# Kernel optimization log

Measured on AMD Instinct MI355X. Metric: run time of the kernel, lower is better.

The kernel has to match this reference:

```python
import jax, jax.numpy as jnp
import numpy as np

# ---- config (matches init_kwargs) ----
B, N_ENC, COND_REPEAT = 4, 4, 200
BLOCKS, LAYERS_PER = 2, 8
R, S, CC, CLASSES = 128, 128, 64, 256
Q_ZERO = 128
DILATIONS = [2 ** i for i in range(LAYERS_PER)] * BLOCKS  # [1..128, 1..128]
L = len(DILATIONS)


def setup_inputs() -> dict:
    key = jax.random.key(0)
    ks = jax.random.split(key, 12)
    g = lambda k, shape, fan: (jax.random.normal(k, shape, jnp.float32) / np.float32(np.sqrt(fan)))
    return {
        "encodings": jax.random.normal(ks[0], (B, CC, N_ENC), jnp.float32),
        "W_first": g(ks[1], (R, 1, 2), 2.0),            # causal conv 1->R, k=2
        "b_first": jnp.zeros((R,), jnp.float32),
        "Wc": g(ks[2], (L, 2 * R, R, 2), 2.0 * R),       # dilated causal convs R->2R, k=2
        "bc": jnp.zeros((L, 2 * R), jnp.float32),
        "Wcond": g(ks[3], (L, 2 * R, CC), CC),           # per-layer 1x1 cond (no bias)
        "Wres": g(ks[4], (L, R, R), R),                  # per-layer 1x1 residual
        "bres": jnp.zeros((L, R), jnp.float32),
        "Wskip_l": g(ks[5], (L, S, R), R),               # per-layer 1x1 skip
        "bskip_l": jnp.zeros((L, S), jnp.float32),
        "Wskip0": g(ks[6], (S, R), R),                   # top skip_conv
        "bskip0": jnp.zeros((S,), jnp.float32),
        "Wcond_top": g(ks[7], (S, CC), CC),              # top 1x1 cond (no bias)
        "Wfc": g(ks[8], (S, S), S),
        "bfc": jnp.zeros((S,), jnp.float32),
        "Wlogits": g(ks[9], (CLASSES, S), S),
        "blogits": jnp.zeros((CLASSES,), jnp.float32),
    }


def reference(encodings, W_first, b_first, Wc, bc, Wcond, Wres, bres,
              Wskip_l, bskip_l, Wskip0, bskip0, Wcond_top, Wfc, bfc,
              Wlogits, blogits):
    """Autoregressive WaveNet generation with per-layer dilated-conv queues.
    Returns per-step logits [B, CLASSES, T] (sampling uses argmax, method='max')."""
    T = N_ENC * COND_REPEAT
    # each encoding frame conditions cond_repeat consecutive samples
    c_seq = jnp.repeat(encodings, COND_REPEAT, axis=2).transpose(2, 0, 1)  # [T,B,CC]

    def step(carry, c_t):
        sample, fq, queues = carry  # sample:[B] int, fq:[B] (first-conv queue), queues: tuple of [B,R,d_l]
        x = sample.astype(jnp.float32) / 127.5 - 1.0  # mu-law index -> [-1, 1]
        # first causal conv (k=2): past value from queue, current value x
        res = fq[:, None] * W_first[:, 0, 0] + x[:, None] * W_first[:, 0, 1] + b_first  # [B,R]
        skip = res @ Wskip0.T + bskip0  # [B,S]
        new_queues = []
        for l in range(L):  # fixed structural loop over layers
            q = queues[l]  # [B,R,d_l]; q[:,:,0] is the input from d_l steps ago
            z = q[:, :, 0] @ Wc[l, :, :, 0].T + res @ Wc[l, :, :, 1].T + bc[l]  # [B,2R]
            z = z + c_t @ Wcond[l].T
            gate, out = jnp.split(z, 2, axis=1)
            h = jax.nn.sigmoid(gate) * jnp.tanh(out)
            new_queues.append(jnp.concatenate([q[:, :, 1:], res[:, :, None]], axis=2))
            skip = skip + h @ Wskip_l[l].T + bskip_l[l]
            res = res + h @ Wres[l].T + bres[l]  # residual connection
        s = jax.nn.relu(skip) @ Wfc.T + bfc + c_t @ Wcond_top.T
        logits = jax.nn.relu(s) @ Wlogits.T + blogits  # [B,CLASSES]
        new_sample = jnp.argmax(logits, axis=1).astype(jnp.int32)
        return (new_sample, x, tuple(new_queues)), logits

    carry0 = (jnp.full((B,), Q_ZERO, jnp.int32),
              jnp.zeros((B,), jnp.float32),
              tuple(jnp.zeros((B, R, d), jnp.float32) for d in DILATIONS))
    _, logits = jax.lax.scan(step, carry0, c_seq)
    return logits.transpose(1, 2, 0)  # [B, CLASSES, T]
```

## Files before the change

kernel.cpp:

```cpp
#include <hip/hip_runtime.h>


typedef unsigned long long u64;

#define TSTEPS 800
#define CREP 200

#define CTR_OFF 0
#define ABT_OFF 64
#define RESBOX_OFF 4096
#define BOXB 16384
#define SKIPBOX_OFF (RESBOX_OFF + 4 * BOXB)
#define RING_OFF (SKIPBOX_OFF + 4 * BOXB)
#define RINGB 261120
#define WS_END (RING_OFF + 4 * RINGB)

#define SPIN_LIMIT 1048576

static __device__ __forceinline__ void pub64(u64* p, float x, unsigned tag) {
  const u64 v = (u64)__float_as_uint(x) | ((u64)tag << 32);
  asm volatile("global_atomic_swap_x2 %0, %1, off" ::"v"(p), "v"(v) : "memory");
}
static __device__ __forceinline__ u64 poll64(u64* p) {
  u64 old;
  const u64 z = 0;
  asm volatile("global_atomic_add_x2 %0, %1, %2, off sc0\n\ts_waitcnt vmcnt(0)"
               : "=&v"(old) : "v"(p), "v"(z) : "memory");
  return old;
}
static __device__ __forceinline__ void poll4(u64* p, u64& a, u64& b, u64& c, u64& d) {
  const u64 z = 0;
  asm volatile(
      "global_atomic_add_x2 %0, %4, %5, off sc0\n\t"
      "global_atomic_add_x2 %1, %4, %5, off offset:1024 sc0\n\t"
      "global_atomic_add_x2 %2, %4, %5, off offset:2048 sc0\n\t"
      "global_atomic_add_x2 %3, %4, %5, off offset:3072 sc0\n\t"
      "s_waitcnt vmcnt(0)"
      : "=&v"(a), "=&v"(b), "=&v"(c), "=&v"(d)
      : "v"(p), "v"(z)
      : "memory");
}
static __device__ __forceinline__ unsigned ld32(const unsigned* p) {
  return __hip_atomic_load(p, __ATOMIC_RELAXED, __HIP_MEMORY_SCOPE_AGENT);
}
static __device__ __forceinline__ void st32(unsigned* p, unsigned v) {
  __hip_atomic_store(p, v, __ATOMIC_RELAXED, __HIP_MEMORY_SCOPE_AGENT);
}
static __device__ __forceinline__ float spinf(u64* p, unsigned tag, unsigned* abt) {
  int g = 0;
  for (;;) {
    const u64 v = poll64(p);
    if ((unsigned)(v >> 32) == tag) return __uint_as_float((unsigned)v);
    if (((++g) & 255) == 0) {
      if (g > SPIN_LIMIT || ld32(abt)) { st32(abt, 1u); return 0.f; }
    }
  }
}

__global__ void wn_init(unsigned char* ws) {
  uint4 z; z.x = 0; z.y = 0; z.z = 0; z.w = 0;
  uint4* p = (uint4*)ws;
  const int n = WS_END / 16;
  for (int i = blockIdx.x * blockDim.x + threadIdx.x; i < n; i += gridDim.x * blockDim.x)
    p[i] = z;
}

__global__ __launch_bounds__(256, 1) void wn_main(
    const float* __restrict__ enc, const float* __restrict__ Wfirst,
    const float* __restrict__ bfirst, const float* __restrict__ Wc,
    const float* __restrict__ bcv, const float* __restrict__ Wcond,
    const float* __restrict__ Wres, const float* __restrict__ bres,
    const float* __restrict__ Wskip, const float* __restrict__ bskipl,
    const float* __restrict__ Wskip0, const float* __restrict__ bskip0,
    const float* __restrict__ Wct, const float* __restrict__ Wfcw,
    const float* __restrict__ bfc, const float* __restrict__ Wlg,
    const float* __restrict__ blgg, float* __restrict__ dout,
    unsigned char* __restrict__ ws) {
  __shared__ __attribute__((aligned(16))) unsigned char smem[8192];
  float* zbS = (float*)smem;
  float* ct2 = (float*)smem;
  float* res0S = (float*)(smem + 2048);
  float* skS = (float*)(smem + 2560);
  float* s1S = (float*)(smem + 3072);
  float* resS = (float*)(smem + 4096);
  float* zS = (float*)(smem + 4608);
  float* hS = (float*)(smem + 5632);
  float* partS = (float*)(smem + 6144);
  float* amaxv = (float*)(smem + 7168);
  int* amaxi = (int*)(smem + 7184);
  int* argixS = (int*)(smem + 7200);
  int* roleS = (int*)(smem + 7216);
  float* pastS = (float*)(smem + 7424);

  const int tid = threadIdx.x;
  unsigned* abt = (unsigned*)(ws + ABT_OFF);

  if (tid == 0) {
    unsigned xcc;
    asm volatile("s_getreg_b32 %0, hwreg(HW_REG_XCC_ID)" : "=s"(xcc));
    int role = 999;
    if (xcc < 4)
      role = (int)__hip_atomic_fetch_add((unsigned*)(ws + CTR_OFF) + xcc, 1u,
                                         __ATOMIC_RELAXED, __HIP_MEMORY_SCOPE_AGENT);
    roleS[0] = role;
    roleS[1] = (int)xcc;
  }
  __syncthreads();
  const int role = roleS[0];
  const int b = roleS[1];
  if (role >= 17) return;

  const int j2 = tid & 127, kh = tid >> 7;

  if (role < 16) {
    const int l = role;
    const int dl = 1 << (l & 7);
    const int pfx = (l < 8) ? ((1 << l) - 1) : (254 + (1 << (l - 8)));

    float wc1r[128], wresr[64];
#pragma unroll
    for (int k = 0; k < 64; k++) {
      const float4 v = ((const float4*)Wc)[(size_t)(l * 256 + tid) * 64 + k];
      wc1r[2 * k] = v.y; wc1r[2 * k + 1] = v.w;
    }
#pragma unroll
    for (int k = 0; k < 16; k++) {
      const float4 v = ((const float4*)(Wres + (size_t)(l * 128 + j2) * 128 + kh * 64))[k];
      wresr[4 * k] = v.x; wresr[4 * k + 1] = v.y; wresr[4 * k + 2] = v.z; wresr[4 * k + 3] = v.w;
    }
    const float bresv = bres[l * 128 + j2];

    for (int e = 0; e < 4; e++) {
      float a = bcv[l * 256 + tid];
      for (int c = 0; c < 64; c++)
        a = fmaf(enc[(b * 64 + c) * 4 + e], Wcond[((size_t)l * 256 + tid) * 64 + c], a);
      zbS[e * 256 + tid] = a;
    }

    u64* inbox = (u64*)(ws + RESBOX_OFF + (size_t)b * BOXB) + l * 128;
    u64* outbox = (u64*)(ws + RESBOX_OFF + (size_t)b * BOXB) + ((l + 1) & 15) * 128;
    u64* skipbox = (u64*)(ws + SKIPBOX_OFF + (size_t)b * BOXB) + l * 128;
    float* ringf = (float*)(ws + RING_OFF + (size_t)b * RINGB) + pfx * 128;
    float pp = 0.f;
    __syncthreads();

    for (int t = 0; t < TSTEPS; t++) {
      const unsigned want = (unsigned)(t + 1);
      const int e = t / CREP;

      if (tid < 128) resS[tid] = spinf(inbox + tid, want, abt);
      __syncthreads();

      float z = pp + zbS[e * 256 + tid];
      {
        const float4* r4 = (const float4*)resS;
#pragma unroll
        for (int k = 0; k < 32; k++) {
          const float4 r = r4[k];
          z = fmaf(r.x, wc1r[4 * k], z);
          z = fmaf(r.y, wc1r[4 * k + 1], z);
          z = fmaf(r.z, wc1r[4 * k + 2], z);
          z = fmaf(r.w, wc1r[4 * k + 3], z);
        }
      }
      zS[tid] = z;
      __syncthreads();
      if (tid < 128) {
        const float g = zS[tid], o = zS[tid + 128];
        hS[tid] = (1.f / (1.f + expf(-g))) * tanhf(o);
      }
      __syncthreads();

      if (l < 15) {
        const float4* h4 = (const float4*)(hS + kh * 64);
        float p = 0.f;
#pragma unroll
        for (int k = 0; k < 16; k++) {
          const float4 hv = h4[k];
          p = fmaf(hv.x, wresr[4 * k], p);
          p = fmaf(hv.y, wresr[4 * k + 1], p);
          p = fmaf(hv.z, wresr[4 * k + 2], p);
          p = fmaf(hv.w, wresr[4 * k + 3], p);
        }
        partS[tid] = p;
        __syncthreads();
        if (tid < 128)
          pub64(outbox + tid, resS[tid] + partS[tid] + partS[tid + 128] + bresv, want);
        __syncthreads();
      }


      {
        const float4* wr = (const float4*)(Wskip + (size_t)(l * 128 + j2) * 128 + kh * 64);
        const float4* h4 = (const float4*)(hS + kh * 64);
        float p = 0.f;
#pragma unroll
        for (int k = 0; k < 16; k++) {
          const float4 wv = wr[k];
          const float4 hv = h4[k];
          p = fmaf(wv.x, hv.x, p);
          p = fmaf(wv.y, hv.y, p);
          p = fmaf(wv.z, hv.z, p);
          p = fmaf(wv.w, hv.w, p);
        }
        partS[tid] = p;
      }
      __syncthreads();
      if (tid < 128) pub64(skipbox + tid, partS[tid] + partS[tid + 128], want);

      if (tid < 128) {
        ringf[(t % dl) * 128 + tid] = resS[tid];
        pastS[tid] = (dl == 1) ? resS[tid] : ringf[((t + 1) % dl) * 128 + tid];
      }
      __syncthreads();
      {
        const float4* wv4 = (const float4*)(Wc + (size_t)(l * 256 + tid) * 256);
        float p2 = 0.f;
#pragma unroll 8
        for (int k = 0; k < 64; k++) {
          const float4 v = wv4[k];
          p2 = fmaf(pastS[2 * k], v.x, p2);
          p2 = fmaf(pastS[2 * k + 1], v.z, p2);
        }
        pp = p2;
      }
    }
  } else {
    float wfcr[64], wlgr[128];
#pragma unroll
    for (int k = 0; k < 16; k++) {
      const float4 v = ((const float4*)(Wfcw + (size_t)j2 * 128 + kh * 64))[k];
      wfcr[4 * k] = v.x; wfcr[4 * k + 1] = v.y; wfcr[4 * k + 2] = v.z; wfcr[4 * k + 3] = v.w;
    }
#pragma unroll
    for (int k = 0; k < 32; k++) {
      const float4 v = ((const float4*)(Wlg + (size_t)tid * 128))[k];
      wlgr[4 * k] = v.x; wlgr[4 * k + 1] = v.y; wlgr[4 * k + 2] = v.z; wlgr[4 * k + 3] = v.w;
    }
    const float wf0 = Wfirst[2 * j2], wf1 = Wfirst[2 * j2 + 1], bfv = bfirst[j2];
    const float bs0 = bskip0[j2];
    float bsum = 0.f;
    for (int l2 = 0; l2 < 16; l2++) bsum += bskipl[l2 * 128 + j2];
    const float bfcv = bfc[j2];
    const float blgv = blgg[tid];
    if (tid < 128) {
      for (int e = 0; e < 4; e++) {
        float a = 0.f;
        for (int c = 0; c < 64; c++)
          a = fmaf(enc[(b * 64 + c) * 4 + e], Wct[tid * 64 + c], a);
        ct2[e * 128 + tid] = a;
      }
    }
    float fq = 0.f, x = 128.f / 127.5f - 1.f;
    u64* res0box = (u64*)(ws + RESBOX_OFF + (size_t)b * BOXB);
    u64* skb = (u64*)(ws + SKIPBOX_OFF + (size_t)b * BOXB);
    __syncthreads();

    for (int t = 0; t < TSTEPS; t++) {
      const unsigned want = (unsigned)(t + 1);
      const int e = t / CREP;

      if (tid < 128) {
        const float rv = fmaf(fq, wf0, fmaf(x, wf1, bfv));
        pub64(res0box + tid, rv, want);
        res0S[tid] = rv;
      }
      __syncthreads();

      {
        const float4* wr = (const float4*)(Wskip0 + (size_t)j2 * 128 + kh * 64);
        const float4* h4 = (const float4*)(res0S + kh * 64);
        float p = 0.f;
#pragma unroll
        for (int k = 0; k < 16; k++) {
          const float4 wv = wr[k];
          const float4 hv = h4[k];
          p = fmaf(wv.x, hv.x, p);
          p = fmaf(wv.y, hv.y, p);
          p = fmaf(wv.z, hv.z, p);
          p = fmaf(wv.w, hv.w, p);
        }
        partS[tid] = p;
      }
      __syncthreads();
      if (tid < 128) {
        float sacc = partS[tid] + partS[tid + 128] + bs0 + bsum;
        u64 v[16];
        int g = 0;
        for (;;) {
          bool ok = true;
#pragma unroll
          for (int grp = 0; grp < 4; grp++)
            poll4(skb + grp * 512 + tid, v[grp * 4], v[grp * 4 + 1], v[grp * 4 + 2], v[grp * 4 + 3]);
#pragma unroll
          for (int l2 = 0; l2 < 16; l2++) ok &= ((unsigned)(v[l2] >> 32) == want);
          if (ok) break;
          if (((++g) & 63) == 0) {
            if (g > (SPIN_LIMIT >> 6) || ld32(abt)) { st32(abt, 1u); break; }
          }
        }
#pragma unroll
        for (int l2 = 0; l2 < 16; l2++) sacc += __uint_as_float((unsigned)v[l2]);
        skS[tid] = fmaxf(sacc, 0.f);
      }
      __syncthreads();

      {
        const float4* h4 = (const float4*)(skS + kh * 64);
        float p = 0.f;
#pragma unroll
        for (int k = 0; k < 16; k++) {
          const float4 hv = h4[k];
          p = fmaf(hv.x, wfcr[4 * k], p);
          p = fmaf(hv.y, wfcr[4 * k + 1], p);
          p = fmaf(hv.z, wfcr[4 * k + 2], p);
          p = fmaf(hv.w, wfcr[4 * k + 3], p);
        }
        partS[tid] = p;
      }
      __syncthreads();
      if (tid < 128)
        s1S[tid] = fmaxf(partS[tid] + partS[tid + 128] + bfcv + ct2[e * 128 + tid], 0.f);
      __syncthreads();

      float lg = blgv;
      {
        const float4* h4 = (const float4*)s1S;
#pragma unroll
        for (int k = 0; k < 32; k++) {
          const float4 hv = h4[k];
          lg = fmaf(hv.x, wlgr[4 * k], lg);
          lg = fmaf(hv.y, wlgr[4 * k + 1], lg);
          lg = fmaf(hv.z, wlgr[4 * k + 2], lg);
          lg = fmaf(hv.w, wlgr[4 * k + 3], lg);
        }
      }

      float bv = lg;
      int bi = tid;
#pragma unroll
      for (int off = 32; off >= 1; off >>= 1) {
        const float ov = __shfl_down(bv, (unsigned)off);
        const int oi = __shfl_down(bi, (unsigned)off);
        if (ov > bv || (ov == bv && oi < bi)) { bv = ov; bi = oi; }
      }
      if ((tid & 63) == 0) { amaxv[tid >> 6] = bv; amaxi[tid >> 6] = bi; }
      __syncthreads();
      if (tid == 0) {
        float bb = amaxv[0];
        int ii = amaxi[0];
        for (int w2 = 1; w2 < 4; w2++)
          if (amaxv[w2] > bb || (amaxv[w2] == bb && amaxi[w2] < ii)) { bb = amaxv[w2]; ii = amaxi[w2]; }
        argixS[0] = ii;
      }
      __syncthreads();
      fq = x;
      x = (float)argixS[0] / 127.5f - 1.f;

      dout[((size_t)b * 256 + tid) * TSTEPS + t] = lg;
    }
  }
}

extern "C" void kernel_launch(void* const* d_in, const int* in_sizes, int n_in,
                              void* d_out, int out_size, void* d_ws, size_t ws_size,
                              hipStream_t stream) {
  (void)in_sizes; (void)n_in; (void)out_size; (void)ws_size;
  wn_init<<<256, 256, 0, stream>>>((unsigned char*)d_ws);
  wn_main<<<1024, 256, 0, stream>>>(
      (const float*)d_in[0], (const float*)d_in[1], (const float*)d_in[2],
      (const float*)d_in[3], (const float*)d_in[4], (const float*)d_in[5],
      (const float*)d_in[6], (const float*)d_in[7], (const float*)d_in[8],
      (const float*)d_in[9], (const float*)d_in[10], (const float*)d_in[11],
      (const float*)d_in[12], (const float*)d_in[13], (const float*)d_in[14],
      (const float*)d_in[15], (const float*)d_in[16],
      (float*)d_out, (unsigned char*)d_ws);
}
```

Baseline: 27.39 ms.

## Double block size to 512 threads and split all matvecs across more threads

Each persistent block now runs 512 threads instead of 256. Every per-step matrix-vector product (dilated conv taps, residual, skip, fc, logits) is split across more threads with partial sums reduced in shared memory. The past-tap weights (wc0) now stay in registers instead of being re-read from global memory every step, and Wskip0 moves into registers as well. The goal is a shorter serial critical path per timestep in this latency-bound pipeline. The cost is extra shared-memory reduction passes and synchronisation, and in the layer roles an added barrier before the residual publish.

```diff
diff --git a/kernel.cpp b/kernel.cpp
--- a/kernel.cpp
+++ b/kernel.cpp
@@ -65,7 +65,7 @@
     p[i] = z;
 }
 
-__global__ __launch_bounds__(256, 1) void wn_main(
+__global__ __launch_bounds__(512, 2) void wn_main(
     const float* __restrict__ enc, const float* __restrict__ Wfirst,
     const float* __restrict__ bfirst, const float* __restrict__ Wc,
     const float* __restrict__ bcv, const float* __restrict__ Wcond,
@@ -76,21 +76,20 @@
     const float* __restrict__ bfc, const float* __restrict__ Wlg,
     const float* __restrict__ blgg, float* __restrict__ dout,
     unsigned char* __restrict__ ws) {
-  __shared__ __attribute__((aligned(16))) unsigned char smem[8192];
+  __shared__ __attribute__((aligned(16))) unsigned char smem[14336];
   float* zbS = (float*)smem;
   float* ct2 = (float*)smem;
-  float* res0S = (float*)(smem + 2048);
-  float* skS = (float*)(smem + 2560);
-  float* s1S = (float*)(smem + 3072);
   float* resS = (float*)(smem + 4096);
-  float* zS = (float*)(smem + 4608);
-  float* hS = (float*)(smem + 5632);
-  float* partS = (float*)(smem + 6144);
-  float* amaxv = (float*)(smem + 7168);
-  int* amaxi = (int*)(smem + 7184);
-  int* argixS = (int*)(smem + 7200);
-  int* roleS = (int*)(smem + 7216);
-  float* pastS = (float*)(smem + 7424);
+  float* zpartS = (float*)(smem + 4608);
+  float* ppS = (float*)(smem + 6656);
+  float* hS = (float*)(smem + 8704);
+  float* rpartS = (float*)(smem + 9216);
+  float* skpartS = (float*)(smem + 11264);
+  float* pastS = (float*)(smem + 13312);
+  float* amaxv = (float*)(smem + 13824);
+  int* amaxi = (int*)(smem + 13840);
+  int* argixS = (int*)(smem + 13856);
+  int* roleS = (int*)(smem + 13872);
 
   const int tid = threadIdx.x;
   unsigned* abt = (unsigned*)(ws + ABT_OFF);
@@ -110,38 +109,48 @@
   const int b = roleS[1];
   if (role >= 17) return;
 
-  const int j2 = tid & 127, kh = tid >> 7;
+  const int jz = tid & 255, kh = tid >> 8;
+  const int j3 = tid & 127, q3 = tid >> 7;
 
   if (role < 16) {
     const int l = role;
     const int dl = 1 << (l & 7);
     const int pfx = (l < 8) ? ((1 << l) - 1) : (254 + (1 << (l - 8)));
 
-    float wc1r[128], wresr[64];
-#pragma unroll
-    for (int k = 0; k < 64; k++) {
-      const float4 v = ((const float4*)Wc)[(size_t)(l * 256 + tid) * 64 + k];
-      wc1r[2 * k] = v.y; wc1r[2 * k + 1] = v.w;
-    }
-#pragma unroll
-    for (int k = 0; k < 16; k++) {
-      const float4 v = ((const float4*)(Wres + (size_t)(l * 128 + j2) * 128 + kh * 64))[k];
-      wresr[4 * k] = v.x; wresr[4 * k + 1] = v.y; wresr[4 * k + 2] = v.z; wresr[4 * k + 3] = v.w;
-    }
-    const float bresv = bres[l * 128 + j2];
-
-    for (int e = 0; e < 4; e++) {
-      float a = bcv[l * 256 + tid];
-      for (int c = 0; c < 64; c++)
-        a = fmaf(enc[(b * 64 + c) * 4 + e], Wcond[((size_t)l * 256 + tid) * 64 + c], a);
-      zbS[e * 256 + tid] = a;
-    }
+    float wc1h[64], wc0h[64], wresq[32];
+    {
+      const float4* wbase = (const float4*)(Wc + ((size_t)(l * 256 + jz) * 128 + kh * 64) * 2);
+#pragma unroll
+      for (int m = 0; m < 32; m++) {
+        const float4 v = wbase[m];
+        wc0h[2 * m] = v.x; wc1h[2 * m] = v.y;
+        wc0h[2 * m + 1] = v.z; wc1h[2 * m + 1] = v.w;
+      }
+      const float4* rbase = (const float4*)(Wres + (size_t)(l * 128 + j3) * 128 + q3 * 32);
+#pragma unroll
+      for (int m = 0; m < 8; m++) {
+        const float4 v = rbase[m];
+        wresq[4 * m] = v.x; wresq[4 * m + 1] = v.y;
+        wresq[4 * m + 2] = v.z; wresq[4 * m + 3] = v.w;
+      }
+    }
+    const float bresv = bres[l * 128 + j3];
+
+    if (tid < 256) {
+      for (int e = 0; e < 4; e++) {
+        float a = bcv[l * 256 + tid];
+        for (int c = 0; c < 64; c++)
+          a = fmaf(enc[(b * 64 + c) * 4 + e], Wcond[((size_t)l * 256 + tid) * 64 + c], a);
+        zbS[e * 256 + tid] = a;
+      }
+    }
+    ppS[tid] = 0.f;
 
     u64* inbox = (u64*)(ws + RESBOX_OFF + (size_t)b * BOXB) + l * 128;
     u64* outbox = (u64*)(ws + RESBOX_OFF + (size_t)b * BOXB) + ((l + 1) & 15) * 128;
     u64* skipbox = (u64*)(ws + SKIPBOX_OFF + (size_t)b * BOXB) + l * 128;
     float* ringf = (float*)(ws + RING_OFF + (size_t)b * RINGB) + pfx * 128;
-    float pp = 0.f;
+    const float4* wskb = (const float4*)(Wskip + (size_t)(l * 128 + j3) * 128 + q3 * 32);
     __syncthreads();
 
     for (int t = 0; t < TSTEPS; t++) {
@@ -151,62 +160,55 @@
       if (tid < 128) resS[tid] = spinf(inbox + tid, want, abt);
       __syncthreads();
 
-      float z = pp + zbS[e * 256 + tid];
-      {
-        const float4* r4 = (const float4*)resS;
-#pragma unroll
-        for (int k = 0; k < 32; k++) {
-          const float4 r = r4[k];
-          z = fmaf(r.x, wc1r[4 * k], z);
-          z = fmaf(r.y, wc1r[4 * k + 1], z);
-          z = fmaf(r.z, wc1r[4 * k + 2], z);
-          z = fmaf(r.w, wc1r[4 * k + 3], z);
+      {
+        const float* rp = resS + kh * 64;
+        float zp = 0.f;
+#pragma unroll
+        for (int kk = 0; kk < 64; kk++) zp = fmaf(rp[kk], wc1h[kk], zp);
+        zpartS[(kh << 8) | jz] = zp;
+      }
+      __syncthreads();
+      if (tid < 128) {
+        const float g0 = zpartS[tid] + zpartS[256 + tid] + ppS[tid] + ppS[256 + tid] +
+                         zbS[e * 256 + tid];
+        const float o0 = zpartS[128 + tid] + zpartS[384 + tid] + ppS[128 + tid] +
+                         ppS[384 + tid] + zbS[e * 256 + 128 + tid];
+        hS[tid] = (1.f / (1.f + expf(-g0))) * tanhf(o0);
+      }
+      __syncthreads();
+
+      {
+        const float* hp = hS + q3 * 32;
+        float rp2 = 0.f;
+#pragma unroll
+        for (int kk = 0; kk < 32; kk++) rp2 = fmaf(hp[kk], wresq[kk], rp2);
+        rpartS[(q3 << 7) | j3] = rp2;
+      }
+      __syncthreads();
+      if (l < 15 && tid < 128)
+        pub64(outbox + tid,
+              resS[tid] + rpartS[tid] + rpartS[128 + tid] + rpartS[256 + tid] +
+                  rpartS[384 + tid] + bresv,
+              want);
+
+      {
+        const float* hp = hS + q3 * 32;
+        float sp = 0.f;
+#pragma unroll
+        for (int m = 0; m < 8; m++) {
+          const float4 wv = wskb[m];
+          sp = fmaf(hp[4 * m], wv.x, sp);
+          sp = fmaf(hp[4 * m + 1], wv.y, sp);
+          sp = fmaf(hp[4 * m + 2], wv.z, sp);
+          sp = fmaf(hp[4 * m + 3], wv.w, sp);
         }
-      }
-      zS[tid] = z;
-      __syncthreads();
-      if (tid < 128) {
-        const float g = zS[tid], o = zS[tid + 128];
-        hS[tid] = (1.f / (1.f + expf(-g))) * tanhf(o);
-      }
-      __syncthreads();
-
-      if (l < 15) {
-        const float4* h4 = (const float4*)(hS + kh * 64);
-        float p = 0.f;
-#pragma unroll
-        for (int k = 0; k < 16; k++) {
-          const float4 hv = h4[k];
-          p = fmaf(hv.x, wresr[4 * k], p);
-          p = fmaf(hv.y, wresr[4 * k + 1], p);
-          p = fmaf(hv.z, wresr[4 * k + 2], p);
-          p = fmaf(hv.w, wresr[4 * k + 3], p);
-        }
-        partS[tid] = p;
-        __syncthreads();
-        if (tid < 128)
-          pub64(outbox + tid, resS[tid] + partS[tid] + partS[tid + 128] + bresv, want);
-        __syncthreads();
-      }
-
-
-      {
-        const float4* wr = (const float4*)(Wskip + (size_t)(l * 128 + j2) * 128 + kh * 64);
-        const float4* h4 = (const float4*)(hS + kh * 64);
-        float p = 0.f;
-#pragma unroll
-        for (int k = 0; k < 16; k++) {
-          const float4 wv = wr[k];
-          const float4 hv = h4[k];
-          p = fmaf(wv.x, hv.x, p);
-          p = fmaf(wv.y, hv.y, p);
-          p = fmaf(wv.z, hv.z, p);
-          p = fmaf(wv.w, hv.w, p);
-        }
-        partS[tid] = p;
-      }
-      __syncthreads();
-      if (tid < 128) pub64(skipbox + tid, partS[tid] + partS[tid + 128], want);
+        skpartS[(q3 << 7) | j3] = sp;
+      }
+      __syncthreads();
+      if (tid < 128)
+        pub64(skipbox + tid,
+              skpartS[tid] + skpartS[128 + tid] + skpartS[256 + tid] + skpartS[384 + tid],
+              want);
 
       if (tid < 128) {
         ringf[(t % dl) * 128 + tid] = resS[tid];
@@ -214,36 +216,41 @@
       }
       __syncthreads();
       {
-        const float4* wv4 = (const float4*)(Wc + (size_t)(l * 256 + tid) * 256);
-        float p2 = 0.f;
-#pragma unroll 8
-        for (int k = 0; k < 64; k++) {
-          const float4 v = wv4[k];
-          p2 = fmaf(pastS[2 * k], v.x, p2);
-          p2 = fmaf(pastS[2 * k + 1], v.z, p2);
-        }
-        pp = p2;
+        const float* pp2 = pastS + kh * 64;
+        float ppn = 0.f;
+#pragma unroll
+        for (int kk = 0; kk < 64; kk++) ppn = fmaf(pp2[kk], wc0h[kk], ppn);
+        ppS[(kh << 8) | jz] = ppn;
       }
     }
   } else {
-    float wfcr[64], wlgr[128];
-#pragma unroll
-    for (int k = 0; k < 16; k++) {
-      const float4 v = ((const float4*)(Wfcw + (size_t)j2 * 128 + kh * 64))[k];
-      wfcr[4 * k] = v.x; wfcr[4 * k + 1] = v.y; wfcr[4 * k + 2] = v.z; wfcr[4 * k + 3] = v.w;
-    }
-#pragma unroll
-    for (int k = 0; k < 32; k++) {
-      const float4 v = ((const float4*)(Wlg + (size_t)tid * 128))[k];
-      wlgr[4 * k] = v.x; wlgr[4 * k + 1] = v.y; wlgr[4 * k + 2] = v.z; wlgr[4 * k + 3] = v.w;
-    }
-    const float wf0 = Wfirst[2 * j2], wf1 = Wfirst[2 * j2 + 1], bfv = bfirst[j2];
-    const float bs0 = bskip0[j2];
-    float bsum = 0.f;
-    for (int l2 = 0; l2 < 16; l2++) bsum += bskipl[l2 * 128 + j2];
-    const float bfcv = bfc[j2];
-    const float blgv = blgg[tid];
+    float wlgr[64], wfcr[32], wsk0[32];
+    {
+      const float4* lb = (const float4*)(Wlg + (size_t)jz * 128 + kh * 64);
+#pragma unroll
+      for (int m = 0; m < 16; m++) {
+        const float4 v = lb[m];
+        wlgr[4 * m] = v.x; wlgr[4 * m + 1] = v.y;
+        wlgr[4 * m + 2] = v.z; wlgr[4 * m + 3] = v.w;
+      }
+      const float4* fb = (const float4*)(Wfcw + (size_t)j3 * 128 + q3 * 32);
+      const float4* sb = (const float4*)(Wskip0 + (size_t)j3 * 128 + q3 * 32);
+#pragma unroll
+      for (int m = 0; m < 8; m++) {
+        const float4 v = fb[m];
+        const float4 u = sb[m];
+        wfcr[4 * m] = v.x; wfcr[4 * m + 1] = v.y;
+        wfcr[4 * m + 2] = v.z; wfcr[4 * m + 3] = v.w;
+        wsk0[4 * m] = u.x; wsk0[4 * m + 1] = u.y;
+        wsk0[4 * m + 2] = u.z; wsk0[4 * m + 3] = u.w;
+      }
+    }
+    float wf0 = 0.f, wf1 = 0.f, bfv = 0.f, bs0 = 0.f, bsum = 0.f, bfcv = 0.f;
     if (tid < 128) {
+      wf0 = Wfirst[2 * tid]; wf1 = Wfirst[2 * tid + 1]; bfv = bfirst[tid];
+      bs0 = bskip0[tid];
+      for (int l2 = 0; l2 < 16; l2++) bsum += bskipl[l2 * 128 + tid];
+      bfcv = bfc[tid];
       for (int e = 0; e < 4; e++) {
         float a = 0.f;
         for (int c = 0; c < 64; c++)
@@ -251,9 +258,15 @@
         ct2[e * 128 + tid] = a;
       }
     }
+    const float blgv = (tid < 256) ? blgg[tid] : 0.f;
     float fq = 0.f, x = 128.f / 127.5f - 1.f;
     u64* res0box = (u64*)(ws + RESBOX_OFF + (size_t)b * BOXB);
     u64* skb = (u64*)(ws + SKIPBOX_OFF + (size_t)b * BOXB);
+    float* res0S = resS;
+    float* partS = zpartS;
+    float* lgS = ppS;
+    float* skS = hS;
+    float* s1S = rpartS;
     __syncthreads();
 
     for (int t = 0; t < TSTEPS; t++) {
@@ -268,30 +281,24 @@
       __syncthreads();
 
       {
-        const float4* wr = (const float4*)(Wskip0 + (size_t)j2 * 128 + kh * 64);
-        const float4* h4 = (const float4*)(res0S + kh * 64);
-        float p = 0.f;
-#pragma unroll
-        for (int k = 0; k < 16; k++) {
-          const float4 wv = wr[k];
-          const float4 hv = h4[k];
-          p = fmaf(wv.x, hv.x, p);
-          p = fmaf(wv.y, hv.y, p);
-          p = fmaf(wv.z, hv.z, p);
-          p = fmaf(wv.w, hv.w, p);
-        }
-        partS[tid] = p;
+        const float* rp = res0S + q3 * 32;
+        float sp = 0.f;
+#pragma unroll
+        for (int kk = 0; kk < 32; kk++) sp = fmaf(rp[kk], wsk0[kk], sp);
+        partS[tid] = sp;
       }
       __syncthreads();
       if (tid < 128) {
-        float sacc = partS[tid] + partS[tid + 128] + bs0 + bsum;
+        float sacc = partS[tid] + partS[128 + tid] + partS[256 + tid] + partS[384 + tid] +
+                     bs0 + bsum;
         u64 v[16];
         int g = 0;
         for (;;) {
           bool ok = true;
 #pragma unroll
           for (int grp = 0; grp < 4; grp++)
-            poll4(skb + grp * 512 + tid, v[grp * 4], v[grp * 4 + 1], v[grp * 4 + 2], v[grp * 4 + 3]);
+            poll4(skb + grp * 512 + tid, v[grp * 4], v[grp * 4 + 1], v[grp * 4 + 2],
+                  v[grp * 4 + 3]);
 #pragma unroll
           for (int l2 = 0; l2 < 16; l2++) ok &= ((unsigned)(v[l2] >> 32) == want);
           if (ok) break;
@@ -306,58 +313,57 @@
       __syncthreads();
 
       {
-        const float4* h4 = (const float4*)(skS + kh * 64);
+        const float* sp2 = skS + q3 * 32;
         float p = 0.f;
 #pragma unroll
-        for (int k = 0; k < 16; k++) {
-          const float4 hv = h4[k];
-          p = fmaf(hv.x, wfcr[4 * k], p);
-          p = fmaf(hv.y, wfcr[4 * k + 1], p);
-          p = fmaf(hv.z, wfcr[4 * k + 2], p);
-          p = fmaf(hv.w, wfcr[4 * k + 3], p);
+        for (int kk = 0; kk < 32; kk++) p = fmaf(sp2[kk], wfcr[kk], p);
+        partS[tid] = p;
+      }
+      __syncthreads();
+      if (tid < 128)
+        s1S[tid] = fmaxf(partS[tid] + partS[128 + tid] + partS[256 + tid] +
+                             partS[384 + tid] + bfcv + ct2[e * 128 + tid],
+                         0.f);
+      __syncthreads();
+
+      {
+        const float* sp3 = s1S + kh * 64;
+        float p = 0.f;
+#pragma unroll
+        for (int kk = 0; kk < 64; kk++) p = fmaf(sp3[kk], wlgr[kk], p);
+        lgS[(kh << 8) | jz] = p;
+      }
+      __syncthreads();
+
+      float lg = 0.f;
+      if (tid < 256) lg = lgS[tid] + lgS[256 + tid] + blgv;
+
+      {
+        float bv = lg;
+        int bi = tid;
+#pragma unroll
+        for (int off = 32; off >= 1; off >>= 1) {
+          const float ov = __shfl_down(bv, (unsigned)off);
+          const int oi = __shfl_down(bi, (unsigned)off);
+          if (ov > bv || (ov == bv && oi < bi)) { bv = ov; bi = oi; }
         }
-        partS[tid] = p;
-      }
-      __syncthreads();
-      if (tid < 128)
-        s1S[tid] = fmaxf(partS[tid] + partS[tid + 128] + bfcv + ct2[e * 128 + tid], 0.f);
-      __syncthreads();
-
-      float lg = blgv;
-      {
-        const float4* h4 = (const float4*)s1S;
-#pragma unroll
-        for (int k = 0; k < 32; k++) {
-          const float4 hv = h4[k];
-          lg = fmaf(hv.x, wlgr[4 * k], lg);
-          lg = fmaf(hv.y, wlgr[4 * k + 1], lg);
-          lg = fmaf(hv.z, wlgr[4 * k + 2], lg);
-          lg = fmaf(hv.w, wlgr[4 * k + 3], lg);
-        }
-      }
-
-      float bv = lg;
-      int bi = tid;
-#pragma unroll
-      for (int off = 32; off >= 1; off >>= 1) {
-        const float ov = __shfl_down(bv, (unsigned)off);
-        const int oi = __shfl_down(bi, (unsigned)off);
-        if (ov > bv || (ov == bv && oi < bi)) { bv = ov; bi = oi; }
-      }
-      if ((tid & 63) == 0) { amaxv[tid >> 6] = bv; amaxi[tid >> 6] = bi; }
+        if (tid < 256 && (tid & 63) == 0) { amaxv[tid >> 6] = bv; amaxi[tid >> 6] = bi; }
+      }
       __syncthreads();
       if (tid == 0) {
         float bb = amaxv[0];
         int ii = amaxi[0];
         for (int w2 = 1; w2 < 4; w2++)
-          if (amaxv[w2] > bb || (amaxv[w2] == bb && amaxi[w2] < ii)) { bb = amaxv[w2]; ii = amaxi[w2]; }
+          if (amaxv[w2] > bb || (amaxv[w2] == bb && amaxi[w2] < ii)) {
+            bb = amaxv[w2]; ii = amaxi[w2];
+          }
         argixS[0] = ii;
       }
       __syncthreads();
       fq = x;
       x = (float)argixS[0] / 127.5f - 1.f;
 
-      dout[((size_t)b * 256 + tid) * TSTEPS + t] = lg;
+      if (tid < 256) dout[((size_t)b * 256 + tid) * TSTEPS + t] = lg;
     }
   }
 }
@@ -367,7 +373,7 @@
                               hipStream_t stream) {
   (void)in_sizes; (void)n_in; (void)out_size; (void)ws_size;
   wn_init<<<256, 256, 0, stream>>>((unsigned char*)d_ws);
-  wn_main<<<1024, 256, 0, stream>>>(
+  wn_main<<<1024, 512, 0, stream>>>(
       (const float*)d_in[0], (const float*)d_in[1], (const float*)d_in[2],
       (const float*)d_in[3], (const float*)d_in[4], (const float*)d_in[5],
       (const float*)d_in[6], (const float*)d_in[7], (const float*)d_in[8],
```

Measured after the change: 23.72 ms. 1.15x faster.
